# Performance work log

Measured on AMD Instinct MI355X. Metric: run time of the kernel, lower is better.

The kernel has to match this reference:

```python
import jax, jax.numpy as jnp
import numpy as np

BN_EPS = 1e-5


def setup_inputs() -> dict:
    key = jax.random.key(0)
    k1, k2 = jax.random.split(key)
    B, P, S, D = 8, 64, 256, 256
    x = jax.random.normal(k1, (B, P, S, D), dtype=jnp.float32)
    # kaiming_normal_ on (planes, S, S): std = sqrt(2 / fan_in), fan_in = S*S
    std = np.sqrt(2.0 / (S * S)).astype(np.float32)
    weights = jax.random.normal(k2, (P, S, S), dtype=jnp.float32) * std
    gamma = jnp.ones((P,), dtype=jnp.float32)
    beta = jnp.zeros((P,), dtype=jnp.float32)
    return {"x": x, "weights": weights, "gamma": gamma, "beta": beta}


def reference(x, weights, gamma, beta):
    # x: (B, P, S, D); weights: (P, S, S)
    D = x.shape[-1]
    inv_dim = 1.0 / jnp.sqrt(jnp.asarray(D, dtype=x.dtype))
    # scores: (B, P, S, S) = x @ x^T / sqrt(D)
    scores = jnp.einsum('bpsd,bptd->bpst', x, x) * inv_dim
    # weighted reduction over last axis -> (B, P, S, 1)
    red = jnp.sum(scores * weights[None], axis=-1, keepdims=True)
    y = x + red  # residual broadcast over D
    # BatchNorm2d in training mode: per-channel batch stats over (B, S, D)
    mean = jnp.mean(y, axis=(0, 2, 3), keepdims=True)
    var = jnp.var(y, axis=(0, 2, 3), keepdims=True)
    y_hat = (y - mean) * jax.lax.rsqrt(var + BN_EPS)
    return y_hat * gamma[None, :, None, None] + beta[None, :, None, None]
```

## Files before the change

### kernel.cpp

```cpp
#include <hip/hip_runtime.h>

typedef __attribute__((ext_vector_type(8))) short short8;
typedef __attribute__((ext_vector_type(4))) float f32x4;

#define NB 8
#define NP 64
#define NS 256
#define ND 256
#define LSTR 264

__device__ __forceinline__ unsigned short f2bf(float f) {
    unsigned int u = __float_as_uint(f);
    u = (u + 0x7FFFu + ((u >> 16) & 1u)) >> 16;
    return (unsigned short)u;
}

__global__ __launch_bounds__(1024, 4) void k1_gemm_red(
    const float* __restrict__ x, const float* __restrict__ w,
    float* __restrict__ red, float* __restrict__ Sx, float* __restrict__ Sxx)
{
    __shared__ unsigned short Xl[NS * LSTR];
    __shared__ float red_l[4][NS];

    const int t    = threadIdx.x;
    const int lane = t & 63;
    const int wv   = t >> 6;
    const int ib   = wv >> 2;
    const int jb   = wv & 3;
    const int p    = blockIdx.x & 63;
    const int b    = blockIdx.x >> 6;

    const float* xb      = x + (size_t)(b * NP + p) * (NS * ND);
    const size_t rowbase = (size_t)(b * NP + p) * NS;

    #pragma unroll 4
    for (int i = 0; i < 16; ++i) {
        const int row = 16 * i + wv;
        f32x4 v = *reinterpret_cast<const f32x4*>(xb + row * ND + 4 * lane);
        float a = (v.x + v.y) + (v.z + v.w);
        #pragma unroll
        for (int off = 1; off < 64; off <<= 1) a += __shfl_xor(a, off, 64);
        if (lane == 0) Sx[rowbase + row] = a;
        unsigned long long pk =
              (unsigned long long)f2bf(v.x)
            | ((unsigned long long)f2bf(v.y) << 16)
            | ((unsigned long long)f2bf(v.z) << 32)
            | ((unsigned long long)f2bf(v.w) << 48);
        *reinterpret_cast<unsigned long long*>(&Xl[row * LSTR + 4 * lane]) = pk;
    }
    __syncthreads();

    const int qd = lane >> 4;
    const int c  = lane & 15;

    f32x4 acc[4][4] = {};
    #pragma unroll 2
    for (int k0 = 0; k0 < ND; k0 += 32) {
        const int kof = k0 + qd * 8;
        short8 afr[4], bfr[4];
        #pragma unroll
        for (int i = 0; i < 4; ++i)
            afr[i] = *reinterpret_cast<const short8*>(
                &Xl[(64 * ib + 16 * i + c) * LSTR + kof]);
        #pragma unroll
        for (int j = 0; j < 4; ++j)
            bfr[j] = *reinterpret_cast<const short8*>(
                &Xl[(64 * jb + 16 * j + c) * LSTR + kof]);
        #pragma unroll
        for (int i = 0; i < 4; ++i)
            #pragma unroll
            for (int j = 0; j < 4; ++j)
                acc[i][j] = __builtin_amdgcn_mfma_f32_16x16x32_bf16(
                    afr[i], bfr[j], acc[i][j], 0, 0, 0);
    }

    if (ib == jb && qd == (c >> 2)) {
        #pragma unroll
        for (int i = 0; i < 4; ++i)
            Sxx[rowbase + 64 * ib + 16 * i + c] = acc[i][i][c & 3];
    }

    const float* wp = w + (size_t)p * (NS * NS);
    #pragma unroll
    for (int i = 0; i < 4; ++i) {
        #pragma unroll
        for (int r = 0; r < 4; ++r) {
            const int rl = 16 * i + 4 * qd + r;
            const float* wrow = wp + (size_t)(64 * ib + rl) * NS + 64 * jb + c;
            float s = acc[i][0][r] * wrow[0]
                    + acc[i][1][r] * wrow[16]
                    + acc[i][2][r] * wrow[32]
                    + acc[i][3][r] * wrow[48];
            #pragma unroll
            for (int off = 1; off < 16; off <<= 1)
                s += __shfl_xor(s, off, 64);
            if (c == 0) red_l[jb][64 * ib + rl] = s;
        }
    }
    __syncthreads();
    if (t < NS)
        red[rowbase + t] =
            (red_l[0][t] + red_l[1][t] + red_l[2][t] + red_l[3][t]) * 0.0625f;
}

__global__ __launch_bounds__(256) void k2_stats(
    const float* __restrict__ red, const float* __restrict__ Sx,
    const float* __restrict__ Sxx, const float* __restrict__ gamma,
    const float* __restrict__ beta, float* __restrict__ sb)
{
    __shared__ float l1[256], l2[256];
    const int p = blockIdx.x;
    const int t = threadIdx.x;
    float sy = 0.f, syy = 0.f;
    for (int n = t; n < NB * NS; n += 256) {
        int bb = n >> 8, s = n & 255;
        size_t idx = (size_t)(bb * NP + p) * NS + s;
        float r = red[idx], a = Sx[idx], q = Sxx[idx];
        sy  += a + 256.f * r;
        syy += q + 2.f * r * a + 256.f * r * r;
    }
    l1[t] = sy; l2[t] = syy;
    __syncthreads();
    for (int off = 128; off > 0; off >>= 1) {
        if (t < off) { l1[t] += l1[t + off]; l2[t] += l2[t + off]; }
        __syncthreads();
    }
    if (t == 0) {
        const float invN = 1.f / (float)(NB * NS * ND);
        float mean = l1[0] * invN;
        float var  = l2[0] * invN - mean * mean;
        float sc   = gamma[p] * rsqrtf(var + 1e-5f);
        sb[p]      = sc;
        sb[64 + p] = beta[p] - mean * sc;
    }
}

__global__ __launch_bounds__(256) void k3_norm(
    const float* __restrict__ x, const float* __restrict__ red,
    const float* __restrict__ sb, float* __restrict__ out)
{
    const size_t f0 = (size_t)blockIdx.x * 1024 + threadIdx.x;
    #pragma unroll
    for (int k = 0; k < 4; ++k) {
        const size_t f = f0 + (size_t)k * 256;
        f32x4 v = reinterpret_cast<const f32x4*>(x)[f];
        const float r  = red[f >> 6];
        const int   pp = (int)((f >> 14) & 63);
        v = (v + r) * sb[pp] + sb[64 + pp];
        __builtin_nontemporal_store(v, reinterpret_cast<f32x4*>(out) + f);
    }
}

extern "C" void kernel_launch(void* const* d_in, const int* in_sizes, int n_in,
                              void* d_out, int out_size, void* d_ws, size_t ws_size,
                              hipStream_t stream)
{
    const float* x     = (const float*)d_in[0];
    const float* w     = (const float*)d_in[1];
    const float* gamma = (const float*)d_in[2];
    const float* beta  = (const float*)d_in[3];
    float* out = (float*)d_out;

    float* red = (float*)d_ws;
    float* Sx  = red + (size_t)NB * NP * NS;
    float* Sxx = Sx  + (size_t)NB * NP * NS;
    float* sb  = Sxx + (size_t)NB * NP * NS;

    hipLaunchKernelGGL(k1_gemm_red, dim3(NB * NP), dim3(1024), 0, stream,
                       x, w, red, Sx, Sxx);
    hipLaunchKernelGGL(k2_stats, dim3(NP), dim3(256), 0, stream,
                       red, Sx, Sxx, gamma, beta, sb);
    hipLaunchKernelGGL(k3_norm, dim3((NB * NP * NS * ND) / (16 * 256)), dim3(256),
                       0, stream, x, red, sb, out);
}
```

Baseline: 289.0 us.

## Split Gram GEMM over K halves with atomic accumulation and smaller blocks

The K dimension (D) is split into two halves, so twice as many 512-thread blocks each stage a 256x128 bf16 tile in LDS instead of 256x256. This raises occupancy and parallelism. Partial sums for red, Sx and Sxx are combined with atomicAdd into a workspace zeroed by a new kernel. Row sums are now computed with MFMA against a ones vector rather than shuffles, and the output store is no longer nontemporal. The costs are an extra launch, atomic traffic, two reads of each weight tile, and partial-sum rounding into red before the weighting.

```diff
diff --git a/kernel.cpp b/kernel.cpp
--- a/kernel.cpp
+++ b/kernel.cpp
@@ -7,7 +7,8 @@
 #define NP 64
 #define NS 256
 #define ND 256
-#define LSTR 264
+#define KH 128
+#define LSTR 136
 
 __device__ __forceinline__ unsigned short f2bf(float f) {
     unsigned int u = __float_as_uint(f);
@@ -15,7 +16,12 @@
     return (unsigned short)u;
 }
 
-__global__ __launch_bounds__(1024, 4) void k1_gemm_red(
+__global__ __launch_bounds__(256) void k0_zero(float* __restrict__ ws) {
+    reinterpret_cast<f32x4*>(ws)[(size_t)blockIdx.x * 256 + threadIdx.x] =
+        f32x4{0.f, 0.f, 0.f, 0.f};
+}
+
+__global__ __launch_bounds__(512, 4) void k1_gemm_red(
     const float* __restrict__ x, const float* __restrict__ w,
     float* __restrict__ red, float* __restrict__ Sx, float* __restrict__ Sxx)
 {
@@ -25,82 +31,105 @@
     const int t    = threadIdx.x;
     const int lane = t & 63;
     const int wv   = t >> 6;
-    const int ib   = wv >> 2;
-    const int jb   = wv & 3;
     const int p    = blockIdx.x & 63;
-    const int b    = blockIdx.x >> 6;
-
-    const float* xb      = x + (size_t)(b * NP + p) * (NS * ND);
+    const int b    = (blockIdx.x >> 6) & 7;
+    const int kh   = blockIdx.x >> 9;
+
+    const float* xb      = x + (size_t)(b * NP + p) * (NS * ND) + kh * KH;
     const size_t rowbase = (size_t)(b * NP + p) * NS;
 
+    const int r32 = t >> 5;
+    const int c32 = t & 31;
     #pragma unroll 4
     for (int i = 0; i < 16; ++i) {
-        const int row = 16 * i + wv;
-        f32x4 v = *reinterpret_cast<const f32x4*>(xb + row * ND + 4 * lane);
-        float a = (v.x + v.y) + (v.z + v.w);
-        #pragma unroll
-        for (int off = 1; off < 64; off <<= 1) a += __shfl_xor(a, off, 64);
-        if (lane == 0) Sx[rowbase + row] = a;
+        const int row = 16 * i + r32;
+        f32x4 v = *reinterpret_cast<const f32x4*>(xb + (size_t)row * ND + 4 * c32);
         unsigned long long pk =
               (unsigned long long)f2bf(v.x)
             | ((unsigned long long)f2bf(v.y) << 16)
             | ((unsigned long long)f2bf(v.z) << 32)
             | ((unsigned long long)f2bf(v.w) << 48);
-        *reinterpret_cast<unsigned long long*>(&Xl[row * LSTR + 4 * lane]) = pk;
+        *reinterpret_cast<unsigned long long*>(&Xl[row * LSTR + 4 * c32]) = pk;
     }
     __syncthreads();
 
     const int qd = lane >> 4;
     const int c  = lane & 15;
 
-    f32x4 acc[4][4] = {};
-    #pragma unroll 2
-    for (int k0 = 0; k0 < ND; k0 += 32) {
-        const int kof = k0 + qd * 8;
-        short8 afr[4], bfr[4];
+    {
+        const short8 ones = {0x3F80, 0x3F80, 0x3F80, 0x3F80,
+                             0x3F80, 0x3F80, 0x3F80, 0x3F80};
         #pragma unroll
-        for (int i = 0; i < 4; ++i)
-            afr[i] = *reinterpret_cast<const short8*>(
-                &Xl[(64 * ib + 16 * i + c) * LSTR + kof]);
-        #pragma unroll
-        for (int j = 0; j < 4; ++j)
-            bfr[j] = *reinterpret_cast<const short8*>(
-                &Xl[(64 * jb + 16 * j + c) * LSTR + kof]);
-        #pragma unroll
-        for (int i = 0; i < 4; ++i)
-            #pragma unroll
-            for (int j = 0; j < 4; ++j)
-                acc[i][j] = __builtin_amdgcn_mfma_f32_16x16x32_bf16(
-                    afr[i], bfr[j], acc[i][j], 0, 0, 0);
-    }
-
-    if (ib == jb && qd == (c >> 2)) {
-        #pragma unroll
-        for (int i = 0; i < 4; ++i)
-            Sxx[rowbase + 64 * ib + 16 * i + c] = acc[i][i][c & 3];
+        for (int h = 0; h < 2; ++h) {
+            const int m = wv + 8 * h;
+            f32x4 sacc = {0.f, 0.f, 0.f, 0.f};
+            #pragma unroll
+            for (int k0 = 0; k0 < KH; k0 += 32) {
+                short8 afr = *reinterpret_cast<const short8*>(
+                    &Xl[(16 * m + c) * LSTR + k0 + qd * 8]);
+                sacc = __builtin_amdgcn_mfma_f32_16x16x32_bf16(afr, ones, sacc, 0, 0, 0);
+            }
+            if (c == 0) {
+                #pragma unroll
+                for (int r = 0; r < 4; ++r)
+                    atomicAdd(&Sx[rowbase + 16 * m + 4 * qd + r], sacc[r]);
+            }
+        }
     }
 
     const float* wp = w + (size_t)p * (NS * NS);
     #pragma unroll
-    for (int i = 0; i < 4; ++i) {
+    for (int pp = 0; pp < 2; ++pp) {
+        const int ib = (wv >> 2) * 2 + pp;
+        const int jb = wv & 3;
+        f32x4 acc[4][4] = {};
         #pragma unroll
-        for (int r = 0; r < 4; ++r) {
-            const int rl = 16 * i + 4 * qd + r;
-            const float* wrow = wp + (size_t)(64 * ib + rl) * NS + 64 * jb + c;
-            float s = acc[i][0][r] * wrow[0]
-                    + acc[i][1][r] * wrow[16]
-                    + acc[i][2][r] * wrow[32]
-                    + acc[i][3][r] * wrow[48];
-            #pragma unroll
-            for (int off = 1; off < 16; off <<= 1)
-                s += __shfl_xor(s, off, 64);
-            if (c == 0) red_l[jb][64 * ib + rl] = s;
+        for (int k0 = 0; k0 < KH; k0 += 32) {
+            const int kof = k0 + qd * 8;
+            short8 afr[4], bfr[4];
+            #pragma unroll
+            for (int i = 0; i < 4; ++i)
+                afr[i] = *reinterpret_cast<const short8*>(
+                    &Xl[(64 * ib + 16 * i + c) * LSTR + kof]);
+            #pragma unroll
+            for (int j = 0; j < 4; ++j)
+                bfr[j] = *reinterpret_cast<const short8*>(
+                    &Xl[(64 * jb + 16 * j + c) * LSTR + kof]);
+            #pragma unroll
+            for (int i = 0; i < 4; ++i)
+                #pragma unroll
+                for (int j = 0; j < 4; ++j)
+                    acc[i][j] = __builtin_amdgcn_mfma_f32_16x16x32_bf16(
+                        afr[i], bfr[j], acc[i][j], 0, 0, 0);
+        }
+
+        if (ib == jb && qd == (c >> 2)) {
+            #pragma unroll
+            for (int i = 0; i < 4; ++i)
+                atomicAdd(&Sxx[rowbase + 64 * ib + 16 * i + c], acc[i][i][c & 3]);
+        }
+
+        #pragma unroll
+        for (int i = 0; i < 4; ++i) {
+            #pragma unroll
+            for (int r = 0; r < 4; ++r) {
+                const int rl = 16 * i + 4 * qd + r;
+                const float* wrow = wp + (size_t)(64 * ib + rl) * NS + 64 * jb + c;
+                float s = acc[i][0][r] * wrow[0]
+                        + acc[i][1][r] * wrow[16]
+                        + acc[i][2][r] * wrow[32]
+                        + acc[i][3][r] * wrow[48];
+                #pragma unroll
+                for (int off = 1; off < 16; off <<= 1)
+                    s += __shfl_xor(s, off, 64);
+                if (c == 0) red_l[jb][64 * ib + rl] = s;
+            }
         }
     }
     __syncthreads();
     if (t < NS)
-        red[rowbase + t] =
-            (red_l[0][t] + red_l[1][t] + red_l[2][t] + red_l[3][t]) * 0.0625f;
+        atomicAdd(&red[rowbase + t],
+                  (red_l[0][t] + red_l[1][t] + red_l[2][t] + red_l[3][t]) * 0.0625f);
 }
 
 __global__ __launch_bounds__(256) void k2_stats(
@@ -147,7 +176,7 @@
         const float r  = red[f >> 6];
         const int   pp = (int)((f >> 14) & 63);
         v = (v + r) * sb[pp] + sb[64 + pp];
-        __builtin_nontemporal_store(v, reinterpret_cast<f32x4*>(out) + f);
+        reinterpret_cast<f32x4*>(out)[f] = v;
     }
 }
 
@@ -166,7 +195,8 @@
     float* Sxx = Sx  + (size_t)NB * NP * NS;
     float* sb  = Sxx + (size_t)NB * NP * NS;
 
-    hipLaunchKernelGGL(k1_gemm_red, dim3(NB * NP), dim3(1024), 0, stream,
+    hipLaunchKernelGGL(k0_zero, dim3(384), dim3(256), 0, stream, red);
+    hipLaunchKernelGGL(k1_gemm_red, dim3(2 * NB * NP), dim3(512), 0, stream,
                        x, w, red, Sx, Sxx);
     hipLaunchKernelGGL(k2_stats, dim3(NP), dim3(256), 0, stream,
                        red, Sx, Sxx, gamma, beta, sb);
```

After: 320.2 us. 1.11x slower.
